# Kernel optimization log

Measured on AMD Instinct MI355X. Metric: run time of the kernel, lower is better.

Reference implementation:

```python
import jax, jax.numpy as jnp
import numpy as np

L, D, H, F, B, S = 6, 1024, 16, 4096, 4, 2048
HD = D // H
EPS = 1e-5
THRESH = 0.93


def setup_inputs() -> dict:
    key = jax.random.key(0)
    ks = jax.random.split(key, 12)
    w = lambda k, shape: jax.random.normal(k, shape, jnp.float32) * 0.02
    return {
        'x': jax.random.normal(ks[0], (B, S, D), jnp.float32),
        'Wq': w(ks[1], (L, D, D)), 'bq': jnp.zeros((L, D), jnp.float32),
        'Wk': w(ks[2], (L, D, D)), 'bk': jnp.zeros((L, D), jnp.float32),
        'Wv': w(ks[3], (L, D, D)), 'bv': jnp.zeros((L, D), jnp.float32),
        'Wo': w(ks[4], (L, D, D)), 'bo': jnp.zeros((L, D), jnp.float32),
        'W1': w(ks[5], (L, D, F)), 'b1': jnp.zeros((L, F), jnp.float32),
        'W2': w(ks[6], (L, F, D)), 'b2': jnp.zeros((L, D), jnp.float32),
        'ln1_g': jnp.ones((L, D), jnp.float32), 'ln1_b': jnp.zeros((L, D), jnp.float32),
        'ln2_g': jnp.ones((L, D), jnp.float32), 'ln2_b': jnp.zeros((L, D), jnp.float32),
        'cW': w(ks[7], (L, D)), 'cb': jnp.zeros((L,), jnp.float32),
    }


def _layernorm(x, g, b):
    m = jnp.mean(x, axis=-1, keepdims=True)
    v = jnp.var(x, axis=-1, keepdims=True)
    return (x - m) * jax.lax.rsqrt(v + EPS) * g + b


def _forward(x, Wq, bq, Wk, bk, Wv, bv, Wo, bo, W1, b1, W2, b2,
             ln1_g, ln1_b, ln2_g, ln2_b, cW, cb):
    Bb, Ss, Dd = x.shape
    scale = HD ** -0.5
    # causal mask: triu(ones(S, S_full), diagonal=S_full-S+1) with no cache -> k=1
    mask = jnp.triu(jnp.ones((Ss, Ss), bool), k=1)  # True where masked

    def step(carry, params):
        xc, done, depth = carry
        i, wq, bq_, wk, bk_, wv, bv_, wo, bo_, w1, b1_, w2, b2_, g1, be1, g2, be2, cw, cb_ = params
        xn = _layernorm(xc, g1, be1)
        q = (xn @ wq + bq_).reshape(Bb, Ss, H, HD).transpose(0, 2, 1, 3)  # bhsd
        k = (xn @ wk + bk_).reshape(Bb, Ss, H, HD).transpose(0, 2, 1, 3)
        v = (xn @ wv + bv_).reshape(Bb, Ss, H, HD).transpose(0, 2, 1, 3)
        attn = jnp.einsum('bhqd,bhkd->bhqk', q, k) * scale
        attn = jnp.where(mask[None, None], -jnp.inf, attn)
        attn = jax.nn.softmax(attn, axis=-1)
        o = jnp.einsum('bhqk,bhkd->bhqd', attn, v).transpose(0, 2, 1, 3).reshape(Bb, Ss, Dd)
        x1 = xc + (o @ wo + bo_)
        x2 = x1 + (jax.nn.relu(_layernorm(x1, g2, be2) @ w1 + b1_) @ w2 + b2_)
        # confidence: AdaptiveAvgPool1d over seq -> Linear(D,1) -> sigmoid -> mean over batch
        conf = jnp.mean(jax.nn.sigmoid(jnp.mean(x2, axis=1) @ cw + cb_))
        x_next = jnp.where(done, xc, x2)
        trigger = jnp.logical_and(jnp.logical_and(~done, i >= 1), conf > THRESH)
        depth = jnp.where(trigger, i + 1, depth)
        done = jnp.logical_or(done, trigger)
        return (x_next, done, depth), None

    xs = (jnp.arange(L, dtype=jnp.int32), Wq, bq, Wk, bk, Wv, bv, Wo, bo,
          W1, b1, W2, b2, ln1_g, ln1_b, ln2_g, ln2_b, cW, cb)
    (x_out, _, depth), _ = jax.lax.scan(step, (x, jnp.array(False), jnp.int32(L)), xs)
    return x_out, depth


def reference(x, Wq, bq, Wk, bk, Wv, bv, Wo, bo, W1, b1, W2, b2,
              ln1_g, ln1_b, ln2_g, ln2_b, cW, cb):
    return _forward(x, Wq, bq, Wk, bk, Wv, bv, Wo, bo, W1, b1, W2, b2,
                    ln1_g, ln1_b, ln2_g, ln2_b, cW, cb)
```

## Files before the change

### kernel.cpp

```cpp
#include <hip/hip_runtime.h>
#include <hip/hip_bf16.h>

#define LL 6
#define DD 1024
#define HH 16
#define HDIM 64
#define FF 4096
#define BB 4
#define SS 2048
#define MM (BB * SS)

using f32x4 = __attribute__((ext_vector_type(4))) float;
using s16x8 = __attribute__((ext_vector_type(8))) short;
using s16x4 = __attribute__((ext_vector_type(4))) short;

static __device__ __forceinline__ short f2bf(float x) {
    unsigned u = __float_as_uint(x);
    u = u + 0x7fffu + ((u >> 16) & 1u);
    return (short)(u >> 16);
}

static __device__ __forceinline__ void gl_lds16(const short* g, short* l) {
    __builtin_amdgcn_global_load_lds(
        (const __attribute__((address_space(1))) void*)g,
        (__attribute__((address_space(3))) void*)l, 16, 0, 0);
}

__global__ void init_k(int* flags) { flags[0] = 0; flags[1] = LL; }

__global__ void write_depth_k(float* out, const int* flags) { out[0] = (float)flags[1]; }

__global__ __launch_bounds__(256) void transpose_w(
    const float* __restrict__ in, short* __restrict__ out, int R, int C,
    const int* __restrict__ done)
{
    if (*done) return;
    __shared__ float t[32][33];
    const int tx = threadIdx.x & 31, ty = threadIdx.x >> 5;
    const int r0 = blockIdx.y * 32, c0 = blockIdx.x * 32;
#pragma unroll
    for (int j = 0; j < 32; j += 8)
        t[ty + j][tx] = in[(size_t)(r0 + ty + j) * C + c0 + tx];
    __syncthreads();
#pragma unroll
    for (int j = 0; j < 32; j += 8)
        out[(size_t)(c0 + ty + j) * R + r0 + tx] = f2bf(t[tx][ty + j]);
}

__global__ __launch_bounds__(256) void layernorm_k(
    const float* __restrict__ x, const float* __restrict__ g, const float* __restrict__ b,
    short* __restrict__ out, const int* __restrict__ done)
{
    if (*done) return;
    const int row = blockIdx.x, tid = threadIdx.x;
    const f32x4 v = *(const f32x4*)(x + (size_t)row * DD + tid * 4);
    float s  = v[0] + v[1] + v[2] + v[3];
    float sq = v[0]*v[0] + v[1]*v[1] + v[2]*v[2] + v[3]*v[3];
#pragma unroll
    for (int m = 1; m < 64; m <<= 1) { s += __shfl_xor(s, m, 64); sq += __shfl_xor(sq, m, 64); }
    __shared__ float red[8];
    if ((tid & 63) == 0) { red[tid >> 6] = s; red[4 + (tid >> 6)] = sq; }
    __syncthreads();
    s  = red[0] + red[1] + red[2] + red[3];
    sq = red[4] + red[5] + red[6] + red[7];
    const float mean = s * (1.f / DD);
    const float rstd = rsqrtf(sq * (1.f / DD) - mean * mean + 1e-5f);
    const f32x4 gg = *(const f32x4*)(g + tid * 4);
    const f32x4 bb = *(const f32x4*)(b + tid * 4);
    s16x4 o;
#pragma unroll
    for (int j = 0; j < 4; ++j) o[j] = f2bf((v[j] - mean) * rstd * gg[j] + bb[j]);
    *(s16x4*)(out + (size_t)row * DD + tid * 4) = o;
}

template<int EPI>
__global__ __launch_bounds__(256) void gemm_bt(
    const short* __restrict__ A, const short* __restrict__ Bt,
    const float* __restrict__ bias,
    short* __restrict__ Cb, float* __restrict__ Cf,
    int M, int N, int K, const int* __restrict__ done)
{
    if (*done) return;
    __shared__ __align__(16) short As[128 * 32];
    __shared__ __align__(16) short Bs[128 * 32];
    const int tid = threadIdx.x;
    const int lane = tid & 63;
    const int wave = tid >> 6;
    const int wr = (wave >> 1) * 64, wc = (wave & 1) * 64;
    const int row0 = blockIdx.y * 128, col0 = blockIdx.x * 128;
    const int r0c = tid >> 2,        k0c = (tid & 3) * 8;
    const int r1c = (256 + tid) >> 2, k1c = (tid & 3) * 8;
    short* dstA0 = As + (size_t)(wave * 64) * 8;
    short* dstA1 = As + (size_t)(256 + wave * 64) * 8;
    short* dstB0 = Bs + (size_t)(wave * 64) * 8;
    short* dstB1 = Bs + (size_t)(256 + wave * 64) * 8;
    f32x4 acc[4][4] = {};
    for (int kt = 0; kt < K; kt += 32) {
        gl_lds16(A  + (size_t)(row0 + r0c) * K + kt + k0c, dstA0);
        gl_lds16(A  + (size_t)(row0 + r1c) * K + kt + k1c, dstA1);
        gl_lds16(Bt + (size_t)(col0 + r0c) * K + kt + k0c, dstB0);
        gl_lds16(Bt + (size_t)(col0 + r1c) * K + kt + k1c, dstB1);
        __syncthreads();
        s16x8 af[4], bfr[4];
#pragma unroll
        for (int m = 0; m < 4; ++m)
            af[m] = *(const s16x8*)&As[(wr + m * 16 + (lane & 15)) * 32 + (lane >> 4) * 8];
#pragma unroll
        for (int n = 0; n < 4; ++n)
            bfr[n] = *(const s16x8*)&Bs[(wc + n * 16 + (lane & 15)) * 32 + (lane >> 4) * 8];
#pragma unroll
        for (int m = 0; m < 4; ++m)
#pragma unroll
            for (int n = 0; n < 4; ++n)
                acc[m][n] = __builtin_amdgcn_mfma_f32_16x16x32_bf16(af[m], bfr[n], acc[m][n], 0, 0, 0);
        __syncthreads();
    }
#pragma unroll
    for (int m = 0; m < 4; ++m) {
        const int row = row0 + wr + m * 16 + (lane >> 4) * 4;
#pragma unroll
        for (int n = 0; n < 4; ++n) {
            const int col = col0 + wc + n * 16 + (lane & 15);
            const float bcol = bias[col];
            if (EPI == 3) {
                const int bh = (row >> 11) * HH + (col >> 6);
                const int d = col & 63, s = row & 2047;
                s16x4 o;
#pragma unroll
                for (int i = 0; i < 4; ++i) o[i] = f2bf(acc[m][n][i] + bcol);
                *(s16x4*)(Cb + ((size_t)bh * 64 + d) * SS + s) = o;
            } else {
#pragma unroll
                for (int i = 0; i < 4; ++i) {
                    const float v = acc[m][n][i] + bcol;
                    const size_t idx = (size_t)(row + i) * N + col;
                    if (EPI == 0)      Cb[idx] = f2bf(v);
                    else if (EPI == 1) Cb[idx] = f2bf(v > 0.f ? v : 0.f);
                    else               Cf[idx] = Cf[idx] + v;
                }
            }
        }
    }
}

__global__ __launch_bounds__(256) void attn_k(
    const short* __restrict__ Q, const short* __restrict__ Kk, const short* __restrict__ Vt_g,
    short* __restrict__ O, const int* __restrict__ done)
{
    if (*done) return;
    __shared__ __align__(16) short Ks[64][72];
    __shared__ __align__(16) short Vs[64][72];
    __shared__ __align__(16) short Pl[4][32][72];
    const int tid = threadIdx.x, lane = tid & 63, wave = tid >> 6;
    const int bh = blockIdx.y, b = bh >> 4, h = bh & 15;
    const size_t headoff = (size_t)b * SS * DD + h * HDIM;
    const size_t vhead = (size_t)bh * 64 * SS;
    const float sc = 0.125f * 1.44269504089f;
    const int r2 = tid >> 3, k2 = (tid & 7) * 8;
    const int rvA = tid >> 3, cvA = (tid & 7) * 8;
    const int rvB = 32 + rvA;
    for (int half = 0; half < 2; ++half) {
        const int qtile = half ? (15 - blockIdx.x) : blockIdx.x;
        const int qblock = qtile * 128;
        const int q0 = qblock + wave * 32;
        s16x8 qf[2][2];
#pragma unroll
        for (int m = 0; m < 2; ++m)
#pragma unroll
            for (int d0 = 0; d0 < 2; ++d0)
                qf[m][d0] = *(const s16x8*)(Q + headoff +
                    (size_t)(q0 + m * 16 + (lane & 15)) * DD + d0 * 32 + (lane >> 4) * 8);
        f32x4 oacc[2][4] = {};
        float mrow[2][4], lrow[2][4];
#pragma unroll
        for (int m = 0; m < 2; ++m)
#pragma unroll
            for (int i = 0; i < 4; ++i) { mrow[m][i] = -__builtin_inff(); lrow[m][i] = 0.f; }
        const int jend = qblock + 64;
        for (int jb = 0; jb <= jend; jb += 64) {
            *(s16x8*)&Ks[r2][k2]      = *(const s16x8*)(Kk + headoff + (size_t)(jb + r2) * DD + k2);
            *(s16x8*)&Ks[r2 + 32][k2] = *(const s16x8*)(Kk + headoff + (size_t)(jb + r2 + 32) * DD + k2);
            *(s16x8*)&Vs[rvA][cvA]    = *(const s16x8*)(Vt_g + vhead + (size_t)rvA * SS + jb + cvA);
            *(s16x8*)&Vs[rvB][cvA]    = *(const s16x8*)(Vt_g + vhead + (size_t)rvB * SS + jb + cvA);
            __syncthreads();
            if (jb <= q0 + 31) {
                const bool needmask = (jb + 63 > q0);
                f32x4 sf[2][4] = {};
#pragma unroll
                for (int n = 0; n < 4; ++n)
#pragma unroll
                    for (int d0 = 0; d0 < 2; ++d0) {
                        const s16x8 kf = *(const s16x8*)&Ks[n * 16 + (lane & 15)][d0 * 32 + (lane >> 4) * 8];
#pragma unroll
                        for (int m = 0; m < 2; ++m)
                            sf[m][n] = __builtin_amdgcn_mfma_f32_16x16x32_bf16(qf[m][d0], kf, sf[m][n], 0, 0, 0);
                    }
#pragma unroll
                for (int m = 0; m < 2; ++m) {
                    float tmax[4] = {-__builtin_inff(), -__builtin_inff(), -__builtin_inff(), -__builtin_inff()};
#pragma unroll
                    for (int n = 0; n < 4; ++n)
#pragma unroll
                        for (int i = 0; i < 4; ++i) {
                            float s = sf[m][n][i] * sc;
                            if (needmask) {
                                const int kv = jb + n * 16 + (lane & 15);
                                const int qr = q0 + m * 16 + (lane >> 4) * 4 + i;
                                if (kv > qr) s = -1e30f;
                            }
                            sf[m][n][i] = s;
                            tmax[i] = fmaxf(tmax[i], s);
                        }
#pragma unroll
                    for (int i = 0; i < 4; ++i) {
#pragma unroll
                        for (int mk = 1; mk < 16; mk <<= 1)
                            tmax[i] = fmaxf(tmax[i], __shfl_xor(tmax[i], mk, 64));
                        const float mnew = fmaxf(mrow[m][i], tmax[i]);
                        const float alpha = exp2f(mrow[m][i] - mnew);
                        mrow[m][i] = mnew;
                        lrow[m][i] *= alpha;
#pragma unroll
                        for (int df = 0; df < 4; ++df) oacc[m][df][i] *= alpha;
                    }
                    float psum[4] = {0.f, 0.f, 0.f, 0.f};
#pragma unroll
                    for (int n = 0; n < 4; ++n)
#pragma unroll
                        for (int i = 0; i < 4; ++i) {
                            const float p = exp2f(sf[m][n][i] - mrow[m][i]);
                            psum[i] += p;
                            Pl[wave][m * 16 + (lane >> 4) * 4 + i][n * 16 + (lane & 15)] = f2bf(p);
                        }
#pragma unroll
                    for (int i = 0; i < 4; ++i) {
#pragma unroll
                        for (int mk = 1; mk < 16; mk <<= 1) psum[i] += __shfl_xor(psum[i], mk, 64);
                        lrow[m][i] += psum[i];
                    }
                }
#pragma unroll
                for (int ks = 0; ks < 2; ++ks) {
                    s16x8 pa[2];
#pragma unroll
                    for (int m = 0; m < 2; ++m)
                        pa[m] = *(const s16x8*)&Pl[wave][m * 16 + (lane & 15)][ks * 32 + (lane >> 4) * 8];
#pragma unroll
                    for (int df = 0; df < 4; ++df) {
                        const s16x8 vbf = *(const s16x8*)&Vs[df * 16 + (lane & 15)][ks * 32 + (lane >> 4) * 8];
#pragma unroll
                        for (int m = 0; m < 2; ++m)
                            oacc[m][df] = __builtin_amdgcn_mfma_f32_16x16x32_bf16(pa[m], vbf, oacc[m][df], 0, 0, 0);
                    }
                }
            }
            __syncthreads();
        }
#pragma unroll
        for (int m = 0; m < 2; ++m)
#pragma unroll
            for (int i = 0; i < 4; ++i) {
                const int qr = q0 + m * 16 + (lane >> 4) * 4 + i;
                const float inv = 1.f / lrow[m][i];
#pragma unroll
                for (int df = 0; df < 4; ++df)
                    O[headoff + (size_t)qr * DD + df * 16 + (lane & 15)] = f2bf(oacc[m][df][i] * inv);
            }
    }
}

__global__ void zero_colsum(float* cs, const int* done) {
    if (*done) return;
    cs[blockIdx.x * 256 + threadIdx.x] = 0.f;
}

__global__ __launch_bounds__(256) void colsum_k(
    const float* __restrict__ x, float* __restrict__ cs, const int* __restrict__ done)
{
    if (*done) return;
    const int d = (blockIdx.x & 3) * 256 + threadIdx.x;
    const int b = blockIdx.x >> 2;
    const int s0 = blockIdx.y * 128;
    float s = 0.f;
    for (int i = 0; i < 128; ++i) s += x[(size_t)(b * SS + s0 + i) * DD + d];
    atomicAdd(&cs[b * DD + d], s);
}

__global__ __launch_bounds__(256) void conf_k(
    const float* __restrict__ colsum, const float* __restrict__ cW, const float* __restrict__ cb,
    int layer, int* __restrict__ flags)
{
    if (flags[0]) return;
    const int tid = threadIdx.x;
    __shared__ float red[4][4];
    float dot[4];
#pragma unroll
    for (int b = 0; b < 4; ++b) {
        float p = 0.f;
        for (int d = tid; d < DD; d += 256) p += colsum[b * DD + d] * cW[d];
#pragma unroll
        for (int m = 1; m < 64; m <<= 1) p += __shfl_xor(p, m, 64);
        dot[b] = p;
    }
    if ((tid & 63) == 0) {
#pragma unroll
        for (int b = 0; b < 4; ++b) red[b][tid >> 6] = dot[b];
    }
    __syncthreads();
    if (tid == 0) {
        float conf = 0.f;
#pragma unroll
        for (int b = 0; b < 4; ++b) {
            const float db = (red[b][0] + red[b][1] + red[b][2] + red[b][3]) * (1.f / SS) + cb[0];
            conf += 1.f / (1.f + expf(-db));
        }
        conf *= 0.25f;
        if (layer >= 1 && conf > 0.93f) { flags[0] = 1; flags[1] = layer + 1; }
    }
}

extern "C" void kernel_launch(void* const* d_in, const int* in_sizes, int n_in,
                              void* d_out, int out_size, void* d_ws, size_t ws_size,
                              hipStream_t stream)
{
    const float* x_in = (const float*)d_in[0];
    const float* Wq  = (const float*)d_in[1];
    const float* bq  = (const float*)d_in[2];
    const float* Wk  = (const float*)d_in[3];
    const float* bk  = (const float*)d_in[4];
    const float* Wv  = (const float*)d_in[5];
    const float* bv  = (const float*)d_in[6];
    const float* Wo  = (const float*)d_in[7];
    const float* bo  = (const float*)d_in[8];
    const float* W1  = (const float*)d_in[9];
    const float* b1  = (const float*)d_in[10];
    const float* W2  = (const float*)d_in[11];
    const float* b2  = (const float*)d_in[12];
    const float* g1  = (const float*)d_in[13];
    const float* be1 = (const float*)d_in[14];
    const float* g2  = (const float*)d_in[15];
    const float* be2 = (const float*)d_in[16];
    const float* cW  = (const float*)d_in[17];
    const float* cb  = (const float*)d_in[18];

    char* ws = (char*)d_ws;
    size_t off = 0;
    auto alloc = [&](size_t bytes) -> char* {
        char* p = ws + off;
        off = (off + bytes + 255) & ~(size_t)255;
        return p;
    };
    int*   flags  = (int*)  alloc(256);
    float* colsum = (float*)alloc((size_t)BB * DD * 4);
    short* xn     = (short*)alloc((size_t)MM * DD * 2);
    short* qb     = (short*)alloc((size_t)MM * DD * 2);
    short* kb     = (short*)alloc((size_t)MM * DD * 2);
    short* vt     = (short*)alloc((size_t)MM * DD * 2);
    short* obuf   = (short*)alloc((size_t)MM * DD * 2);
    short* hb     = qb;
    short* wtq    = (short*)alloc((size_t)DD * DD * 2);
    short* wtk    = (short*)alloc((size_t)DD * DD * 2);
    short* wtv    = (short*)alloc((size_t)DD * DD * 2);
    short* wto    = (short*)alloc((size_t)DD * DD * 2);
    short* wt1    = (short*)alloc((size_t)DD * FF * 2);
    short* wt2    = (short*)alloc((size_t)DD * FF * 2);
    (void)ws_size; (void)in_sizes; (void)n_in; (void)out_size;

    float* x = (float*)d_out;

    hipMemcpyAsync(x, x_in, (size_t)MM * DD * 4, hipMemcpyDeviceToDevice, stream);
    init_k<<<1, 1, 0, stream>>>(flags);
    const int* done = flags;

    for (int l = 0; l < LL; ++l) {
        const size_t wdd = (size_t)l * DD * DD;
        const size_t wdf = (size_t)l * DD * FF;
        transpose_w<<<dim3(32, 32), 256, 0, stream>>>(Wq + wdd, wtq, DD, DD, done);
        transpose_w<<<dim3(32, 32), 256, 0, stream>>>(Wk + wdd, wtk, DD, DD, done);
        transpose_w<<<dim3(32, 32), 256, 0, stream>>>(Wv + wdd, wtv, DD, DD, done);
        transpose_w<<<dim3(32, 32), 256, 0, stream>>>(Wo + wdd, wto, DD, DD, done);
        transpose_w<<<dim3(128, 32), 256, 0, stream>>>(W1 + wdf, wt1, DD, FF, done);
        transpose_w<<<dim3(32, 128), 256, 0, stream>>>(W2 + wdf, wt2, FF, DD, done);

        layernorm_k<<<MM, 256, 0, stream>>>(x, g1 + l * DD, be1 + l * DD, xn, done);
        gemm_bt<0><<<dim3(DD / 128, MM / 128), 256, 0, stream>>>(xn, wtq, bq + l * DD, qb, nullptr, MM, DD, DD, done);
        gemm_bt<0><<<dim3(DD / 128, MM / 128), 256, 0, stream>>>(xn, wtk, bk + l * DD, kb, nullptr, MM, DD, DD, done);
        gemm_bt<3><<<dim3(DD / 128, MM / 128), 256, 0, stream>>>(xn, wtv, bv + l * DD, vt, nullptr, MM, DD, DD, done);
        attn_k<<<dim3(8, BB * HH), 256, 0, stream>>>(qb, kb, vt, obuf, done);
        gemm_bt<2><<<dim3(DD / 128, MM / 128), 256, 0, stream>>>(obuf, wto, bo + l * DD, nullptr, x, MM, DD, DD, done);
        layernorm_k<<<MM, 256, 0, stream>>>(x, g2 + l * DD, be2 + l * DD, xn, done);
        gemm_bt<1><<<dim3(FF / 128, MM / 128), 256, 0, stream>>>(xn, wt1, b1 + (size_t)l * FF, hb, nullptr, MM, FF, DD, done);
        gemm_bt<2><<<dim3(DD / 128, MM / 128), 256, 0, stream>>>(hb, wt2, b2 + l * DD, nullptr, x, MM, DD, FF, done);

        zero_colsum<<<16, 256, 0, stream>>>(colsum, done);
        colsum_k<<<dim3(16, 16), 256, 0, stream>>>(x, colsum, done);
        conf_k<<<1, 256, 0, stream>>>(colsum, cW + l * DD, cb + l, l, flags);
    }

    write_depth_k<<<1, 1, 0, stream>>>((float*)d_out + (size_t)MM * DD, flags);
}
```

Measured before the change: 3.612 ms.

## Fuse QKV GEMMs and weight transposes; shrink attention q-tile with MFMA row sums

Merges the six per-layer weight transpose launches into a single kernel and concatenates the Q/K/V weights, so one GEMM launch with a split epilogue produces all three projections. Attention now uses 64-row query tiles, one 16-row slab per wave, over twice as many blocks. It computes softmax row sums with an MFMA against a ones vector instead of shuffle reductions. The aim is fewer launches, better GPU fill and less shuffle work, at the cost of reloading K/V more often per query row and using bf16-rounded probabilities in the normaliser.

```diff
diff --git a/kernel.cpp b/kernel.cpp
--- a/kernel.cpp
+++ b/kernel.cpp
@@ -30,14 +30,35 @@
 
 __global__ void write_depth_k(float* out, const int* flags) { out[0] = (float)flags[1]; }
 
-__global__ __launch_bounds__(256) void transpose_w(
-    const float* __restrict__ in, short* __restrict__ out, int R, int C,
+__global__ __launch_bounds__(256) void transpose_all(
+    const float* __restrict__ Wq, const float* __restrict__ Wk,
+    const float* __restrict__ Wv, const float* __restrict__ Wo,
+    const float* __restrict__ W1f, const float* __restrict__ W2f,
+    short* __restrict__ wqkv, short* __restrict__ wto,
+    short* __restrict__ wt1, short* __restrict__ wt2,
     const int* __restrict__ done)
 {
     if (*done) return;
+    const int bid = blockIdx.x;
+    const float* in; short* out; int R, C, bx, by;
+    if (bid < 3072) {
+        const int wsel = bid >> 10, local = bid & 1023;
+        in = wsel == 0 ? Wq : (wsel == 1 ? Wk : Wv);
+        out = wqkv + (size_t)wsel * DD * DD;
+        R = DD; C = DD; bx = local & 31; by = local >> 5;
+    } else if (bid < 4096) {
+        const int local = bid - 3072;
+        in = Wo; out = wto; R = DD; C = DD; bx = local & 31; by = local >> 5;
+    } else if (bid < 8192) {
+        const int local = bid - 4096;
+        in = W1f; out = wt1; R = DD; C = FF; bx = local & 127; by = local >> 7;
+    } else {
+        const int local = bid - 8192;
+        in = W2f; out = wt2; R = FF; C = DD; bx = local & 31; by = local >> 5;
+    }
     __shared__ float t[32][33];
     const int tx = threadIdx.x & 31, ty = threadIdx.x >> 5;
-    const int r0 = blockIdx.y * 32, c0 = blockIdx.x * 32;
+    const int r0 = by * 32, c0 = bx * 32;
 #pragma unroll
     for (int j = 0; j < 32; j += 8)
         t[ty + j][tx] = in[(size_t)(r0 + ty + j) * C + c0 + tx];
@@ -76,8 +97,9 @@
 template<int EPI>
 __global__ __launch_bounds__(256) void gemm_bt(
     const short* __restrict__ A, const short* __restrict__ Bt,
-    const float* __restrict__ bias,
-    short* __restrict__ Cb, float* __restrict__ Cf,
+    const float* __restrict__ b0, const float* __restrict__ b1, const float* __restrict__ b2,
+    short* __restrict__ Cq, short* __restrict__ Ck, short* __restrict__ Cv,
+    float* __restrict__ Cf,
     int M, int N, int K, const int* __restrict__ done)
 {
     if (*done) return;
@@ -115,27 +137,38 @@
                 acc[m][n] = __builtin_amdgcn_mfma_f32_16x16x32_bf16(af[m], bfr[n], acc[m][n], 0, 0, 0);
         __syncthreads();
     }
+    const int sel = col0 >> 10;
+    const float* bp = (EPI == 4) ? (sel == 0 ? b0 : (sel == 1 ? b1 : b2)) : b0;
 #pragma unroll
     for (int m = 0; m < 4; ++m) {
         const int row = row0 + wr + m * 16 + (lane >> 4) * 4;
 #pragma unroll
         for (int n = 0; n < 4; ++n) {
             const int col = col0 + wc + n * 16 + (lane & 15);
-            const float bcol = bias[col];
-            if (EPI == 3) {
-                const int bh = (row >> 11) * HH + (col >> 6);
-                const int d = col & 63, s = row & 2047;
-                s16x4 o;
-#pragma unroll
-                for (int i = 0; i < 4; ++i) o[i] = f2bf(acc[m][n][i] + bcol);
-                *(s16x4*)(Cb + ((size_t)bh * 64 + d) * SS + s) = o;
+            if (EPI == 4) {
+                const int colq = col & 1023;
+                const float bcol = bp[colq];
+                if (sel < 2) {
+                    short* dst = sel == 0 ? Cq : Ck;
+#pragma unroll
+                    for (int i = 0; i < 4; ++i)
+                        dst[(size_t)(row + i) * DD + colq] = f2bf(acc[m][n][i] + bcol);
+                } else {
+                    const int bh = (row >> 11) * HH + (colq >> 6);
+                    const int d = colq & 63, s = row & 2047;
+                    s16x4 o;
+#pragma unroll
+                    for (int i = 0; i < 4; ++i) o[i] = f2bf(acc[m][n][i] + bcol);
+                    *(s16x4*)(Cv + ((size_t)bh * 64 + d) * SS + s) = o;
+                }
             } else {
+                const float bcol = bp[col];
 #pragma unroll
                 for (int i = 0; i < 4; ++i) {
                     const float v = acc[m][n][i] + bcol;
                     const size_t idx = (size_t)(row + i) * N + col;
-                    if (EPI == 0)      Cb[idx] = f2bf(v);
-                    else if (EPI == 1) Cb[idx] = f2bf(v > 0.f ? v : 0.f);
+                    if (EPI == 0)      Cq[idx] = f2bf(v);
+                    else if (EPI == 1) Cq[idx] = f2bf(v > 0.f ? v : 0.f);
                     else               Cf[idx] = Cf[idx] + v;
                 }
             }
@@ -150,7 +183,7 @@
     if (*done) return;
     __shared__ __align__(16) short Ks[64][72];
     __shared__ __align__(16) short Vs[64][72];
-    __shared__ __align__(16) short Pl[4][32][72];
+    __shared__ __align__(16) short Pl[4][16][72];
     const int tid = threadIdx.x, lane = tid & 63, wave = tid >> 6;
     const int bh = blockIdx.y, b = bh >> 4, h = bh & 15;
     const size_t headoff = (size_t)b * SS * DD + h * HDIM;
@@ -159,113 +192,91 @@
     const int r2 = tid >> 3, k2 = (tid & 7) * 8;
     const int rvA = tid >> 3, cvA = (tid & 7) * 8;
     const int rvB = 32 + rvA;
+    s16x8 ones;
+#pragma unroll
+    for (int j = 0; j < 8; ++j) ones[j] = (short)0x3F80;
     for (int half = 0; half < 2; ++half) {
-        const int qtile = half ? (15 - blockIdx.x) : blockIdx.x;
-        const int qblock = qtile * 128;
-        const int q0 = qblock + wave * 32;
-        s16x8 qf[2][2];
-#pragma unroll
-        for (int m = 0; m < 2; ++m)
-#pragma unroll
-            for (int d0 = 0; d0 < 2; ++d0)
-                qf[m][d0] = *(const s16x8*)(Q + headoff +
-                    (size_t)(q0 + m * 16 + (lane & 15)) * DD + d0 * 32 + (lane >> 4) * 8);
-        f32x4 oacc[2][4] = {};
-        float mrow[2][4], lrow[2][4];
-#pragma unroll
-        for (int m = 0; m < 2; ++m)
-#pragma unroll
-            for (int i = 0; i < 4; ++i) { mrow[m][i] = -__builtin_inff(); lrow[m][i] = 0.f; }
-        const int jend = qblock + 64;
-        for (int jb = 0; jb <= jend; jb += 64) {
+        const int qtile = half ? (31 - blockIdx.x) : blockIdx.x;
+        const int qblock = qtile * 64;
+        const int q0 = qblock + wave * 16;
+        s16x8 qf[2];
+#pragma unroll
+        for (int d0 = 0; d0 < 2; ++d0)
+            qf[d0] = *(const s16x8*)(Q + headoff +
+                (size_t)(q0 + (lane & 15)) * DD + d0 * 32 + (lane >> 4) * 8);
+        f32x4 oacc[4] = {};
+        f32x4 ol = {};
+        float mrow[4];
+#pragma unroll
+        for (int i = 0; i < 4; ++i) mrow[i] = -__builtin_inff();
+        for (int jb = 0; jb <= qblock; jb += 64) {
             *(s16x8*)&Ks[r2][k2]      = *(const s16x8*)(Kk + headoff + (size_t)(jb + r2) * DD + k2);
             *(s16x8*)&Ks[r2 + 32][k2] = *(const s16x8*)(Kk + headoff + (size_t)(jb + r2 + 32) * DD + k2);
             *(s16x8*)&Vs[rvA][cvA]    = *(const s16x8*)(Vt_g + vhead + (size_t)rvA * SS + jb + cvA);
             *(s16x8*)&Vs[rvB][cvA]    = *(const s16x8*)(Vt_g + vhead + (size_t)rvB * SS + jb + cvA);
             __syncthreads();
-            if (jb <= q0 + 31) {
-                const bool needmask = (jb + 63 > q0);
-                f32x4 sf[2][4] = {};
-#pragma unroll
-                for (int n = 0; n < 4; ++n)
-#pragma unroll
-                    for (int d0 = 0; d0 < 2; ++d0) {
-                        const s16x8 kf = *(const s16x8*)&Ks[n * 16 + (lane & 15)][d0 * 32 + (lane >> 4) * 8];
-#pragma unroll
-                        for (int m = 0; m < 2; ++m)
-                            sf[m][n] = __builtin_amdgcn_mfma_f32_16x16x32_bf16(qf[m][d0], kf, sf[m][n], 0, 0, 0);
+            f32x4 sf[4] = {};
+#pragma unroll
+            for (int n = 0; n < 4; ++n)
+#pragma unroll
+                for (int d0 = 0; d0 < 2; ++d0) {
+                    const s16x8 kf = *(const s16x8*)&Ks[n * 16 + (lane & 15)][d0 * 32 + (lane >> 4) * 8];
+                    sf[n] = __builtin_amdgcn_mfma_f32_16x16x32_bf16(qf[d0], kf, sf[n], 0, 0, 0);
+                }
+            const bool needmask = (jb + 63 > q0);
+            float tmax[4] = {-__builtin_inff(), -__builtin_inff(), -__builtin_inff(), -__builtin_inff()};
+#pragma unroll
+            for (int n = 0; n < 4; ++n)
+#pragma unroll
+                for (int i = 0; i < 4; ++i) {
+                    float s = sf[n][i] * sc;
+                    if (needmask) {
+                        const int kv = jb + n * 16 + (lane & 15);
+                        const int qr = q0 + (lane >> 4) * 4 + i;
+                        if (kv > qr) s = -1e30f;
                     }
-#pragma unroll
-                for (int m = 0; m < 2; ++m) {
-                    float tmax[4] = {-__builtin_inff(), -__builtin_inff(), -__builtin_inff(), -__builtin_inff()};
-#pragma unroll
-                    for (int n = 0; n < 4; ++n)
-#pragma unroll
-                        for (int i = 0; i < 4; ++i) {
-                            float s = sf[m][n][i] * sc;
-                            if (needmask) {
-                                const int kv = jb + n * 16 + (lane & 15);
-                                const int qr = q0 + m * 16 + (lane >> 4) * 4 + i;
-                                if (kv > qr) s = -1e30f;
-                            }
-                            sf[m][n][i] = s;
-                            tmax[i] = fmaxf(tmax[i], s);
-                        }
-#pragma unroll
-                    for (int i = 0; i < 4; ++i) {
-#pragma unroll
-                        for (int mk = 1; mk < 16; mk <<= 1)
-                            tmax[i] = fmaxf(tmax[i], __shfl_xor(tmax[i], mk, 64));
-                        const float mnew = fmaxf(mrow[m][i], tmax[i]);
-                        const float alpha = exp2f(mrow[m][i] - mnew);
-                        mrow[m][i] = mnew;
-                        lrow[m][i] *= alpha;
-#pragma unroll
-                        for (int df = 0; df < 4; ++df) oacc[m][df][i] *= alpha;
-                    }
-                    float psum[4] = {0.f, 0.f, 0.f, 0.f};
-#pragma unroll
-                    for (int n = 0; n < 4; ++n)
-#pragma unroll
-                        for (int i = 0; i < 4; ++i) {
-                            const float p = exp2f(sf[m][n][i] - mrow[m][i]);
-                            psum[i] += p;
-                            Pl[wave][m * 16 + (lane >> 4) * 4 + i][n * 16 + (lane & 15)] = f2bf(p);
-                        }
-#pragma unroll
-                    for (int i = 0; i < 4; ++i) {
-#pragma unroll
-                        for (int mk = 1; mk < 16; mk <<= 1) psum[i] += __shfl_xor(psum[i], mk, 64);
-                        lrow[m][i] += psum[i];
-                    }
-                }
-#pragma unroll
-                for (int ks = 0; ks < 2; ++ks) {
-                    s16x8 pa[2];
-#pragma unroll
-                    for (int m = 0; m < 2; ++m)
-                        pa[m] = *(const s16x8*)&Pl[wave][m * 16 + (lane & 15)][ks * 32 + (lane >> 4) * 8];
-#pragma unroll
-                    for (int df = 0; df < 4; ++df) {
-                        const s16x8 vbf = *(const s16x8*)&Vs[df * 16 + (lane & 15)][ks * 32 + (lane >> 4) * 8];
-#pragma unroll
-                        for (int m = 0; m < 2; ++m)
-                            oacc[m][df] = __builtin_amdgcn_mfma_f32_16x16x32_bf16(pa[m], vbf, oacc[m][df], 0, 0, 0);
-                    }
+                    sf[n][i] = s;
+                    tmax[i] = fmaxf(tmax[i], s);
+                }
+#pragma unroll
+            for (int i = 0; i < 4; ++i) {
+#pragma unroll
+                for (int mk = 1; mk < 16; mk <<= 1)
+                    tmax[i] = fmaxf(tmax[i], __shfl_xor(tmax[i], mk, 64));
+                const float mnew = fmaxf(mrow[i], tmax[i]);
+                const float alpha = exp2f(mrow[i] - mnew);
+                mrow[i] = mnew;
+                ol[i] *= alpha;
+#pragma unroll
+                for (int df = 0; df < 4; ++df) oacc[df][i] *= alpha;
+            }
+#pragma unroll
+            for (int n = 0; n < 4; ++n)
+#pragma unroll
+                for (int i = 0; i < 4; ++i) {
+                    const float p = exp2f(sf[n][i] - mrow[i]);
+                    Pl[wave][(lane >> 4) * 4 + i][n * 16 + (lane & 15)] = f2bf(p);
+                }
+#pragma unroll
+            for (int ks = 0; ks < 2; ++ks) {
+                const s16x8 pa = *(const s16x8*)&Pl[wave][lane & 15][ks * 32 + (lane >> 4) * 8];
+                ol = __builtin_amdgcn_mfma_f32_16x16x32_bf16(pa, ones, ol, 0, 0, 0);
+#pragma unroll
+                for (int df = 0; df < 4; ++df) {
+                    const s16x8 vbf = *(const s16x8*)&Vs[df * 16 + (lane & 15)][ks * 32 + (lane >> 4) * 8];
+                    oacc[df] = __builtin_amdgcn_mfma_f32_16x16x32_bf16(pa, vbf, oacc[df], 0, 0, 0);
                 }
             }
             __syncthreads();
         }
 #pragma unroll
-        for (int m = 0; m < 2; ++m)
-#pragma unroll
-            for (int i = 0; i < 4; ++i) {
-                const int qr = q0 + m * 16 + (lane >> 4) * 4 + i;
-                const float inv = 1.f / lrow[m][i];
-#pragma unroll
-                for (int df = 0; df < 4; ++df)
-                    O[headoff + (size_t)qr * DD + df * 16 + (lane & 15)] = f2bf(oacc[m][df][i] * inv);
-            }
+        for (int i = 0; i < 4; ++i) {
+            const int qr = q0 + (lane >> 4) * 4 + i;
+            const float inv = 1.f / ol[i];
+#pragma unroll
+            for (int df = 0; df < 4; ++df)
+                O[headoff + (size_t)qr * DD + df * 16 + (lane & 15)] = f2bf(oacc[df][i] * inv);
+        }
     }
 }
 
@@ -358,9 +369,7 @@
     short* vt     = (short*)alloc((size_t)MM * DD * 2);
     short* obuf   = (short*)alloc((size_t)MM * DD * 2);
     short* hb     = qb;
-    short* wtq    = (short*)alloc((size_t)DD * DD * 2);
-    short* wtk    = (short*)alloc((size_t)DD * DD * 2);
-    short* wtv    = (short*)alloc((size_t)DD * DD * 2);
+    short* wqkv   = (short*)alloc((size_t)3 * DD * DD * 2);
     short* wto    = (short*)alloc((size_t)DD * DD * 2);
     short* wt1    = (short*)alloc((size_t)DD * FF * 2);
     short* wt2    = (short*)alloc((size_t)DD * FF * 2);
@@ -375,22 +384,25 @@
     for (int l = 0; l < LL; ++l) {
         const size_t wdd = (size_t)l * DD * DD;
         const size_t wdf = (size_t)l * DD * FF;
-        transpose_w<<<dim3(32, 32), 256, 0, stream>>>(Wq + wdd, wtq, DD, DD, done);
-        transpose_w<<<dim3(32, 32), 256, 0, stream>>>(Wk + wdd, wtk, DD, DD, done);
-        transpose_w<<<dim3(32, 32), 256, 0, stream>>>(Wv + wdd, wtv, DD, DD, done);
-        transpose_w<<<dim3(32, 32), 256, 0, stream>>>(Wo + wdd, wto, DD, DD, done);
-        transpose_w<<<dim3(128, 32), 256, 0, stream>>>(W1 + wdf, wt1, DD, FF, done);
-        transpose_w<<<dim3(32, 128), 256, 0, stream>>>(W2 + wdf, wt2, FF, DD, done);
+        transpose_all<<<12288, 256, 0, stream>>>(Wq + wdd, Wk + wdd, Wv + wdd, Wo + wdd,
+                                                 W1 + wdf, W2 + wdf,
+                                                 wqkv, wto, wt1, wt2, done);
 
         layernorm_k<<<MM, 256, 0, stream>>>(x, g1 + l * DD, be1 + l * DD, xn, done);
-        gemm_bt<0><<<dim3(DD / 128, MM / 128), 256, 0, stream>>>(xn, wtq, bq + l * DD, qb, nullptr, MM, DD, DD, done);
-        gemm_bt<0><<<dim3(DD / 128, MM / 128), 256, 0, stream>>>(xn, wtk, bk + l * DD, kb, nullptr, MM, DD, DD, done);
-        gemm_bt<3><<<dim3(DD / 128, MM / 128), 256, 0, stream>>>(xn, wtv, bv + l * DD, vt, nullptr, MM, DD, DD, done);
-        attn_k<<<dim3(8, BB * HH), 256, 0, stream>>>(qb, kb, vt, obuf, done);
-        gemm_bt<2><<<dim3(DD / 128, MM / 128), 256, 0, stream>>>(obuf, wto, bo + l * DD, nullptr, x, MM, DD, DD, done);
+        gemm_bt<4><<<dim3(3 * DD / 128, MM / 128), 256, 0, stream>>>(
+            xn, wqkv, bq + l * DD, bk + l * DD, bv + l * DD,
+            qb, kb, vt, nullptr, MM, 3 * DD, DD, done);
+        attn_k<<<dim3(16, BB * HH), 256, 0, stream>>>(qb, kb, vt, obuf, done);
+        gemm_bt<2><<<dim3(DD / 128, MM / 128), 256, 0, stream>>>(
+            obuf, wto, bo + l * DD, nullptr, nullptr,
+            nullptr, nullptr, nullptr, x, MM, DD, DD, done);
         layernorm_k<<<MM, 256, 0, stream>>>(x, g2 + l * DD, be2 + l * DD, xn, done);
-        gemm_bt<1><<<dim3(FF / 128, MM / 128), 256, 0, stream>>>(xn, wt1, b1 + (size_t)l * FF, hb, nullptr, MM, FF, DD, done);
-        gemm_bt<2><<<dim3(DD / 128, MM / 128), 256, 0, stream>>>(hb, wt2, b2 + l * DD, nullptr, x, MM, DD, FF, done);
+        gemm_bt<1><<<dim3(FF / 128, MM / 128), 256, 0, stream>>>(
+            xn, wt1, b1 + (size_t)l * FF, nullptr, nullptr,
+            hb, nullptr, nullptr, nullptr, MM, FF, DD, done);
+        gemm_bt<2><<<dim3(DD / 128, MM / 128), 256, 0, stream>>>(
+            hb, wt2, b2 + l * DD, nullptr, nullptr,
+            nullptr, nullptr, nullptr, x, MM, DD, FF, done);
 
         zero_colsum<<<16, 256, 0, stream>>>(colsum, done);
         colsum_k<<<dim3(16, 16), 256, 0, stream>>>(x, colsum, done);
```

After: 3.255 ms. 1.11x faster.
